# Optimization experiments

Measured on AMD Instinct MI355X. Metric: run time of the kernel, lower is better.

Reference implementation:

```python
import jax, jax.numpy as jnp
import numpy as np

N = 50000       # nodes
E = 800000      # edges
D_IN, D_H, D_OUT = 64, 64, 32


def _glorot(key, fan_in, fan_out):
    lim = np.sqrt(6.0 / (fan_in + fan_out)).astype(np.float32)
    return jax.random.uniform(key, (fan_in, fan_out), jnp.float32, -lim, lim)


def setup_inputs() -> dict:
    key = jax.random.key(0)
    k = jax.random.split(key, 4)
    x = jax.random.normal(k[0], (N, D_IN), jnp.float32)
    edge_index = jax.random.randint(k[1], (2, E), 0, N, dtype=jnp.int64)
    W1 = _glorot(k[2], D_IN, D_H)
    b1 = jnp.zeros((D_H,), jnp.float32)
    W2 = _glorot(k[3], D_H, D_OUT)
    b2 = jnp.zeros((D_OUT,), jnp.float32)
    return {"x": x, "edge_index": edge_index, "W1": W1, "b1": b1, "W2": W2, "b2": b2}


def gcn_layer(x, W, b, src, dst, n):
    # PyG GCNConv: h = XW; add self-loops (weight 1); symmetric normalization
    # out[j] = sum_{i->j} h[i] / sqrt(deg(i) deg(j)) + h[j]/deg(j) + b
    h = x @ W                                           # [n, d_out]
    deg = jax.ops.segment_sum(jnp.ones((src.shape[0],), h.dtype), dst,
                              num_segments=n) + 1.0     # in-degree + self-loop
    dinv = jax.lax.rsqrt(deg)                           # deg >= 1
    norm = (dinv[src] * dinv[dst])[:, None]             # [E, 1]
    agg = jax.ops.segment_sum(h[src] * norm, dst, num_segments=n)
    # self-loop contribution: dinv[i]*dinv[i]*h[i]
    return agg + h * (dinv * dinv)[:, None] + b


def reference(x, edge_index, W1, b1, W2, b2):
    src, dst = edge_index[0], edge_index[1]
    h = gcn_layer(x, W1, b1, src, dst, N)
    h = jax.nn.relu(h)                                  # dropout is identity in eval mode
    return gcn_layer(h, W2, b2, src, dst, N)
```

## Files before the change

### kernel.cpp

```cpp
#include <hip/hip_runtime.h>
#include <hip/hip_fp16.h>
#include <cstddef>
#include <cstdint>

namespace {

constexpr int N  = 50000;
constexpr int E  = 800000;
constexpr int DH = 64;
constexpr int DO = 32;
constexpr int NB = (N + 255) / 256;
static_assert(N < 65536, "src packed as u16");
static_assert(NB <= 256, "phase-B single tile");

__device__ inline uint16_t f2bf(float f) {
    union { float f; uint32_t u; } c; c.f = f;
    uint32_t r = c.u + 0x7FFFu + ((c.u >> 16) & 1u);
    return (uint16_t)(r >> 16);
}
__device__ inline void bf2x(uint32_t p, float& a, float& b) {
    union { uint32_t u; float f; } c0, c1;
    c0.u = p << 16; c1.u = p & 0xFFFF0000u;
    a = c0.f; b = c1.f;
}

__global__ void k_zero(int* __restrict__ cnt) {
    int i = blockIdx.x * blockDim.x + threadIdx.x;
    if (i < N) cnt[i] = 0;
}

__global__ void k_count(const int* __restrict__ dst, int* __restrict__ cnt,
                        int* __restrict__ rank) {
    int e = blockIdx.x * blockDim.x + threadIdx.x;
    if (e < E) rank[e] = atomicAdd(&cnt[dst[e]], 1);
}

__launch_bounds__(256)
__global__ void k_gemm1(const float* __restrict__ X, const float* __restrict__ W1,
                        uint16_t* __restrict__ h1) {
    __shared__ float Ws[64 * DH];
    __shared__ float Xs[64 * 68];

    const int tid = threadIdx.x;
    const int rowBase = blockIdx.x * 64;

#pragma unroll
    for (int i = 0; i < 4; ++i) {
        const int q = tid + i * 256;
        reinterpret_cast<float4*>(Ws)[q] = reinterpret_cast<const float4*>(W1)[q];
    }
#pragma unroll
    for (int i = 0; i < 4; ++i) {
        const int q   = tid + i * 256;
        const int row = q >> 4;
        const int kq  = q & 15;
        const int gr  = min(rowBase + row, N - 1);
        const float4 v = *reinterpret_cast<const float4*>(X + (size_t)gr * 64 + kq * 4);
        *reinterpret_cast<float4*>(&Xs[row * 68 + kq * 4]) = v;
    }
    __syncthreads();

    const int rg = tid >> 4;
    const int cg = tid & 15;
    float acc[4][4];
#pragma unroll
    for (int r = 0; r < 4; ++r)
#pragma unroll
        for (int c = 0; c < 4; ++c) acc[r][c] = 0.0f;

#pragma unroll
    for (int k4 = 0; k4 < 16; ++k4) {
        const int k = k4 * 4;
        float xr[4][4];
#pragma unroll
        for (int r = 0; r < 4; ++r) {
            const float4 v = *reinterpret_cast<const float4*>(&Xs[(rg * 4 + r) * 68 + k]);
            xr[r][0] = v.x; xr[r][1] = v.y; xr[r][2] = v.z; xr[r][3] = v.w;
        }
#pragma unroll
        for (int i = 0; i < 4; ++i) {
            const float4 v = *reinterpret_cast<const float4*>(&Ws[(k + i) * DH + cg * 4]);
            const float wv[4] = {v.x, v.y, v.z, v.w};
#pragma unroll
            for (int r = 0; r < 4; ++r)
#pragma unroll
                for (int c = 0; c < 4; ++c) acc[r][c] += xr[r][i] * wv[c];
        }
    }

#pragma unroll
    for (int r = 0; r < 4; ++r) {
        const int row = rowBase + rg * 4 + r;
        if (row < N) {
            uint2 o;
            o.x = (uint32_t)f2bf(acc[r][0]) | ((uint32_t)f2bf(acc[r][1]) << 16);
            o.y = (uint32_t)f2bf(acc[r][2]) | ((uint32_t)f2bf(acc[r][3]) << 16);
            *reinterpret_cast<uint2*>(&h1[(size_t)row * DH + cg * 4]) = o;
        }
    }
}

__global__ void k_scanA(const int* __restrict__ cnt, int* __restrict__ incl,
                        int* __restrict__ bsum) {
    __shared__ int ts[256];
    const int t = threadIdx.x;
    const int i = blockIdx.x * 256 + t;
    const int v = (i < N) ? cnt[i] : 0;
    ts[t] = v;
    __syncthreads();
#pragma unroll
    for (int off = 1; off < 256; off <<= 1) {
        const int u = (t >= off) ? ts[t - off] : 0;
        __syncthreads();
        ts[t] += u;
        __syncthreads();
    }
    if (i < N) incl[i] = ts[t];
    if (t == 255) bsum[blockIdx.x] = ts[255];
}

__global__ void k_scanB(int* __restrict__ bsum) {
    __shared__ int ts[256];
    const int t = threadIdx.x;
    const int v = (t < NB) ? bsum[t] : 0;
    ts[t] = v;
    __syncthreads();
#pragma unroll
    for (int off = 1; off < 256; off <<= 1) {
        const int u = (t >= off) ? ts[t - off] : 0;
        __syncthreads();
        ts[t] += u;
        __syncthreads();
    }
    if (t < NB) bsum[t] = ts[t] - v;
}

__global__ void k_scanC(const int* __restrict__ cnt, const int* __restrict__ incl,
                        const int* __restrict__ bbase, int* __restrict__ rowptr,
                        float* __restrict__ dinv) {
    const int i = blockIdx.x * 256 + threadIdx.x;
    if (i >= N) return;
    const int c    = cnt[i];
    const int excl = bbase[blockIdx.x] + incl[i] - c;
    rowptr[i] = excl;
    dinv[i]   = rsqrtf((float)(c + 1));
    if (i == N - 1) rowptr[N] = excl + c;
}

__global__ void k_fill(const int* __restrict__ src, const int* __restrict__ dst,
                       const int* __restrict__ rank, const int* __restrict__ rowptr,
                       const float* __restrict__ dinv, uint32_t* __restrict__ epack) {
    int e = blockIdx.x * blockDim.x + threadIdx.x;
    if (e >= E) return;
    const int s = src[e], d = dst[e];
    const int pos = rowptr[d] + rank[e];
    const float wn = dinv[s] * dinv[d];
    const uint16_t hb = __half_as_ushort(__float2half(wn));
    epack[pos] = (uint32_t)s | ((uint32_t)hb << 16);
}

__launch_bounds__(256)
__global__ void k_agg1(const int* __restrict__ rowptr, const uint32_t* __restrict__ epack,
                       const uint16_t* __restrict__ h1, const float* __restrict__ dinv,
                       const float* __restrict__ W2, const float* __restrict__ b1,
                       uint16_t* __restrict__ h2) {
    const int gtid = blockIdx.x * 256 + threadIdx.x;
    const int n    = gtid >> 6;
    const int lane = threadIdx.x & 63;
    if (n >= N) return;
    const int g  = lane >> 3;
    const int sl = lane & 7;

    float w2r[8][4];
#pragma unroll
    for (int k = 0; k < 8; ++k) {
        const float4 v = *reinterpret_cast<const float4*>(W2 + (size_t)(sl * 8 + k) * DO + g * 4);
        w2r[k][0] = v.x; w2r[k][1] = v.y; w2r[k][2] = v.z; w2r[k][3] = v.w;
    }
    float b1r[8];
    {
        const float4 a = *reinterpret_cast<const float4*>(b1 + sl * 8);
        const float4 b = *reinterpret_cast<const float4*>(b1 + sl * 8 + 4);
        b1r[0] = a.x; b1r[1] = a.y; b1r[2] = a.z; b1r[3] = a.w;
        b1r[4] = b.x; b1r[5] = b.y; b1r[6] = b.z; b1r[7] = b.w;
    }

    const int beg = rowptr[n], end = rowptr[n + 1];

    float acc[8] = {0.f, 0.f, 0.f, 0.f, 0.f, 0.f, 0.f, 0.f};
    for (int j = beg; j < end; j += 8) {
        const int jj = j + g;
        int s = 0; float wn = 0.0f;
        if (jj < end) {
            const uint32_t w = epack[jj];
            s  = (int)(w & 0xFFFFu);
            wn = __half2float(__ushort_as_half((uint16_t)(w >> 16)));
        }
        const uint4 v = *reinterpret_cast<const uint4*>(h1 + (size_t)s * DH + sl * 8);
        float f0, f1;
        bf2x(v.x, f0, f1); acc[0] += wn * f0; acc[1] += wn * f1;
        bf2x(v.y, f0, f1); acc[2] += wn * f0; acc[3] += wn * f1;
        bf2x(v.z, f0, f1); acc[4] += wn * f0; acc[5] += wn * f1;
        bf2x(v.w, f0, f1); acc[6] += wn * f0; acc[7] += wn * f1;
    }
#pragma unroll
    for (int m = 8; m < 64; m <<= 1)
#pragma unroll
        for (int k = 0; k < 8; ++k) acc[k] += __shfl_xor(acc[k], m);

    const float di = dinv[n], d2 = di * di;
    const uint4 sv = *reinterpret_cast<const uint4*>(h1 + (size_t)n * DH + sl * 8);
    float y[8];
    {
        float f0, f1;
        bf2x(sv.x, f0, f1); y[0] = acc[0] + f0 * d2; y[1] = acc[1] + f1 * d2;
        bf2x(sv.y, f0, f1); y[2] = acc[2] + f0 * d2; y[3] = acc[3] + f1 * d2;
        bf2x(sv.z, f0, f1); y[4] = acc[4] + f0 * d2; y[5] = acc[5] + f1 * d2;
        bf2x(sv.w, f0, f1); y[6] = acc[6] + f0 * d2; y[7] = acc[7] + f1 * d2;
    }
#pragma unroll
    for (int k = 0; k < 8; ++k) y[k] = fmaxf(y[k] + b1r[k], 0.0f);

    float o[4] = {0.f, 0.f, 0.f, 0.f};
#pragma unroll
    for (int k = 0; k < 8; ++k)
#pragma unroll
        for (int c = 0; c < 4; ++c) o[c] += y[k] * w2r[k][c];
#pragma unroll
    for (int m = 1; m < 8; m <<= 1)
#pragma unroll
        for (int c = 0; c < 4; ++c) o[c] += __shfl_xor(o[c], m);

    if (sl == 0) {
        uint2 pk;
        pk.x = (uint32_t)f2bf(o[0]) | ((uint32_t)f2bf(o[1]) << 16);
        pk.y = (uint32_t)f2bf(o[2]) | ((uint32_t)f2bf(o[3]) << 16);
        *reinterpret_cast<uint2*>(h2 + (size_t)n * DO + g * 4) = pk;
    }
}

__global__ void k_agg2(const int* __restrict__ rowptr, const uint32_t* __restrict__ epack,
                       const uint16_t* __restrict__ h2, const float* __restrict__ dinv,
                       const float* __restrict__ b2, float* __restrict__ out) {
    const int gtid = blockIdx.x * blockDim.x + threadIdx.x;
    const int n    = gtid >> 6;
    const int lane = gtid & 63;
    if (n >= N) return;
    const int g  = lane >> 2;
    const int sl = lane & 3;
    const int beg = rowptr[n], end = rowptr[n + 1];

    float acc[8] = {0.f, 0.f, 0.f, 0.f, 0.f, 0.f, 0.f, 0.f};
    for (int j = beg; j < end; j += 16) {
        const int jj = j + g;
        int s = 0; float wn = 0.0f;
        if (jj < end) {
            const uint32_t w = epack[jj];
            s  = (int)(w & 0xFFFFu);
            wn = __half2float(__ushort_as_half((uint16_t)(w >> 16)));
        }
        const uint4 v = *reinterpret_cast<const uint4*>(h2 + (size_t)s * DO + sl * 8);
        float f0, f1;
        bf2x(v.x, f0, f1); acc[0] += wn * f0; acc[1] += wn * f1;
        bf2x(v.y, f0, f1); acc[2] += wn * f0; acc[3] += wn * f1;
        bf2x(v.z, f0, f1); acc[4] += wn * f0; acc[5] += wn * f1;
        bf2x(v.w, f0, f1); acc[6] += wn * f0; acc[7] += wn * f1;
    }
#pragma unroll
    for (int m = 4; m < 64; m <<= 1)
#pragma unroll
        for (int k = 0; k < 8; ++k) acc[k] += __shfl_xor(acc[k], m);

    if (g < 2) {
        const float di = dinv[n], d2 = di * di;
        const int fb = sl * 8 + g * 4;
        const uint2 sv = *reinterpret_cast<const uint2*>(h2 + (size_t)n * DO + fb);
        float s0, s1, s2, s3;
        bf2x(sv.x, s0, s1); bf2x(sv.y, s2, s3);
        const float4 bv = *reinterpret_cast<const float4*>(b2 + fb);
        float4 o;
        o.x = acc[g * 4 + 0] + s0 * d2 + bv.x;
        o.y = acc[g * 4 + 1] + s1 * d2 + bv.y;
        o.z = acc[g * 4 + 2] + s2 * d2 + bv.z;
        o.w = acc[g * 4 + 3] + s3 * d2 + bv.w;
        *reinterpret_cast<float4*>(out + (size_t)n * DO + fb) = o;
    }
}

template <typename T>
T* alignp(char*& p, size_t count) {
    uintptr_t u = ((uintptr_t)p + 63) & ~(uintptr_t)63;
    p = (char*)(u + count * sizeof(T));
    return (T*)u;
}

}

extern "C" void kernel_launch(void* const* d_in, const int* in_sizes, int n_in,
                              void* d_out, int out_size, void* d_ws, size_t ws_size,
                              hipStream_t stream) {
    const float* x   = (const float*)d_in[0];
    const int*   ei  = (const int*)d_in[1];
    const float* W1  = (const float*)d_in[2];
    const float* b1  = (const float*)d_in[3];
    const float* W2  = (const float*)d_in[4];
    const float* b2  = (const float*)d_in[5];
    float* out = (float*)d_out;

    const int* src = ei;
    const int* dst = ei + E;

    char* p = (char*)d_ws;
    int*      cnt    = alignp<int>(p, N);
    int*      rowptr = alignp<int>(p, N + 1);
    int*      rank   = alignp<int>(p, E);
    float*    dinv   = alignp<float>(p, N);
    int*      incl   = alignp<int>(p, N);
    int*      bsum   = alignp<int>(p, NB);
    uint32_t* epack  = alignp<uint32_t>(p, E);
    uint16_t* h1     = alignp<uint16_t>(p, (size_t)N * DH);
    uint16_t* h2     = alignp<uint16_t>(p, (size_t)N * DO);

    hipLaunchKernelGGL(k_zero, dim3((N + 255) / 256), dim3(256), 0, stream, cnt);
    hipLaunchKernelGGL(k_count, dim3((E + 255) / 256), dim3(256), 0, stream,
                       dst, cnt, rank);
    hipLaunchKernelGGL(k_gemm1, dim3((N + 63) / 64), dim3(256), 0, stream, x, W1, h1);
    hipLaunchKernelGGL(k_scanA, dim3(NB), dim3(256), 0, stream, cnt, incl, bsum);
    hipLaunchKernelGGL(k_scanB, dim3(1), dim3(256), 0, stream, bsum);
    hipLaunchKernelGGL(k_scanC, dim3(NB), dim3(256), 0, stream, cnt, incl, bsum,
                       rowptr, dinv);
    hipLaunchKernelGGL(k_fill, dim3((E + 255) / 256), dim3(256), 0, stream,
                       src, dst, rank, rowptr, dinv, epack);
    hipLaunchKernelGGL(k_agg1, dim3((N * 64 + 255) / 256), dim3(256), 0, stream,
                       rowptr, epack, h1, dinv, W2, b1, h2);
    hipLaunchKernelGGL(k_agg2, dim3((N * 64 + 255) / 256), dim3(256), 0, stream,
                       rowptr, epack, h2, dinv, b2, out);
}
```

Before: 179.0 us.

## Split layer-2 GEMM out of agg1 into a separate tiled kernel

Stops fusing the W2 projection into the first aggregation kernel. agg1 now writes the ReLU activations in fp32 to a new buffer, and a new shared-memory tiled GEMM kernel multiplies them by W2 and writes h2 as bf16. This removes per-wavefront W2 register loads and shuffle reductions from the gather kernel. The cost is a 12.8 MB fp32 intermediate that must be written and read back, plus one more kernel launch.

Result: faster. 152.1 us (-15.0%).

```diff
diff --git a/kernel.cpp b/kernel.cpp
--- a/kernel.cpp
+++ b/kernel.cpp
@@ -96,6 +96,67 @@
             o.x = (uint32_t)f2bf(acc[r][0]) | ((uint32_t)f2bf(acc[r][1]) << 16);
             o.y = (uint32_t)f2bf(acc[r][2]) | ((uint32_t)f2bf(acc[r][3]) << 16);
             *reinterpret_cast<uint2*>(&h1[(size_t)row * DH + cg * 4]) = o;
+        }
+    }
+}
+
+__launch_bounds__(256)
+__global__ void k_gemm2(const float* __restrict__ Y, const float* __restrict__ W2,
+                        uint16_t* __restrict__ h2) {
+    __shared__ float Ws[64 * DO];
+    __shared__ float Xs[64 * 68];
+
+    const int tid = threadIdx.x;
+    const int rowBase = blockIdx.x * 64;
+
+#pragma unroll
+    for (int i = 0; i < 2; ++i) {
+        const int q = tid + i * 256;
+        reinterpret_cast<float4*>(Ws)[q] = reinterpret_cast<const float4*>(W2)[q];
+    }
+#pragma unroll
+    for (int i = 0; i < 4; ++i) {
+        const int q   = tid + i * 256;
+        const int row = q >> 4;
+        const int kq  = q & 15;
+        const int gr  = min(rowBase + row, N - 1);
+        const float4 v = *reinterpret_cast<const float4*>(Y + (size_t)gr * 64 + kq * 4);
+        *reinterpret_cast<float4*>(&Xs[row * 68 + kq * 4]) = v;
+    }
+    __syncthreads();
+
+    const int rg = tid >> 4;
+    const int cg = tid & 15;
+    float acc[4][2];
+#pragma unroll
+    for (int r = 0; r < 4; ++r) { acc[r][0] = 0.0f; acc[r][1] = 0.0f; }
+
+#pragma unroll
+    for (int k4 = 0; k4 < 16; ++k4) {
+        const int k = k4 * 4;
+        float xr[4][4];
+#pragma unroll
+        for (int r = 0; r < 4; ++r) {
+            const float4 v = *reinterpret_cast<const float4*>(&Xs[(rg * 4 + r) * 68 + k]);
+            xr[r][0] = v.x; xr[r][1] = v.y; xr[r][2] = v.z; xr[r][3] = v.w;
+        }
+#pragma unroll
+        for (int i = 0; i < 4; ++i) {
+            const float2 v = *reinterpret_cast<const float2*>(&Ws[(k + i) * DO + cg * 2]);
+#pragma unroll
+            for (int r = 0; r < 4; ++r) {
+                acc[r][0] += xr[r][i] * v.x;
+                acc[r][1] += xr[r][i] * v.y;
+            }
+        }
+    }
+
+#pragma unroll
+    for (int r = 0; r < 4; ++r) {
+        const int row = rowBase + rg * 4 + r;
+        if (row < N) {
+            const uint32_t o = (uint32_t)f2bf(acc[r][0]) | ((uint32_t)f2bf(acc[r][1]) << 16);
+            *reinterpret_cast<uint32_t*>(&h2[(size_t)row * DO + cg * 2]) = o;
         }
     }
 }
@@ -162,29 +223,13 @@
 __launch_bounds__(256)
 __global__ void k_agg1(const int* __restrict__ rowptr, const uint32_t* __restrict__ epack,
                        const uint16_t* __restrict__ h1, const float* __restrict__ dinv,
-                       const float* __restrict__ W2, const float* __restrict__ b1,
-                       uint16_t* __restrict__ h2) {
+                       const float* __restrict__ b1, float* __restrict__ y1) {
     const int gtid = blockIdx.x * 256 + threadIdx.x;
     const int n    = gtid >> 6;
     const int lane = threadIdx.x & 63;
     if (n >= N) return;
     const int g  = lane >> 3;
     const int sl = lane & 7;
-
-    float w2r[8][4];
-#pragma unroll
-    for (int k = 0; k < 8; ++k) {
-        const float4 v = *reinterpret_cast<const float4*>(W2 + (size_t)(sl * 8 + k) * DO + g * 4);
-        w2r[k][0] = v.x; w2r[k][1] = v.y; w2r[k][2] = v.z; w2r[k][3] = v.w;
-    }
-    float b1r[8];
-    {
-        const float4 a = *reinterpret_cast<const float4*>(b1 + sl * 8);
-        const float4 b = *reinterpret_cast<const float4*>(b1 + sl * 8 + 4);
-        b1r[0] = a.x; b1r[1] = a.y; b1r[2] = a.z; b1r[3] = a.w;
-        b1r[4] = b.x; b1r[5] = b.y; b1r[6] = b.z; b1r[7] = b.w;
-    }
-
     const int beg = rowptr[n], end = rowptr[n + 1];
 
     float acc[8] = {0.f, 0.f, 0.f, 0.f, 0.f, 0.f, 0.f, 0.f};
@@ -208,34 +253,19 @@
 #pragma unroll
         for (int k = 0; k < 8; ++k) acc[k] += __shfl_xor(acc[k], m);
 
-    const float di = dinv[n], d2 = di * di;
-    const uint4 sv = *reinterpret_cast<const uint4*>(h1 + (size_t)n * DH + sl * 8);
-    float y[8];
-    {
-        float f0, f1;
-        bf2x(sv.x, f0, f1); y[0] = acc[0] + f0 * d2; y[1] = acc[1] + f1 * d2;
-        bf2x(sv.y, f0, f1); y[2] = acc[2] + f0 * d2; y[3] = acc[3] + f1 * d2;
-        bf2x(sv.z, f0, f1); y[4] = acc[4] + f0 * d2; y[5] = acc[5] + f1 * d2;
-        bf2x(sv.w, f0, f1); y[6] = acc[6] + f0 * d2; y[7] = acc[7] + f1 * d2;
-    }
-#pragma unroll
-    for (int k = 0; k < 8; ++k) y[k] = fmaxf(y[k] + b1r[k], 0.0f);
-
-    float o[4] = {0.f, 0.f, 0.f, 0.f};
-#pragma unroll
-    for (int k = 0; k < 8; ++k)
-#pragma unroll
-        for (int c = 0; c < 4; ++c) o[c] += y[k] * w2r[k][c];
-#pragma unroll
-    for (int m = 1; m < 8; m <<= 1)
-#pragma unroll
-        for (int c = 0; c < 4; ++c) o[c] += __shfl_xor(o[c], m);
-
-    if (sl == 0) {
-        uint2 pk;
-        pk.x = (uint32_t)f2bf(o[0]) | ((uint32_t)f2bf(o[1]) << 16);
-        pk.y = (uint32_t)f2bf(o[2]) | ((uint32_t)f2bf(o[3]) << 16);
-        *reinterpret_cast<uint2*>(h2 + (size_t)n * DO + g * 4) = pk;
+    if (g < 2) {
+        const float di = dinv[n], d2 = di * di;
+        const int fb = sl * 8 + g * 4;
+        const uint2 sv = *reinterpret_cast<const uint2*>(h1 + (size_t)n * DH + fb);
+        float s0, s1, s2, s3;
+        bf2x(sv.x, s0, s1); bf2x(sv.y, s2, s3);
+        const float4 bv = *reinterpret_cast<const float4*>(b1 + fb);
+        float4 o;
+        o.x = fmaxf(acc[g * 4 + 0] + s0 * d2 + bv.x, 0.f);
+        o.y = fmaxf(acc[g * 4 + 1] + s1 * d2 + bv.y, 0.f);
+        o.z = fmaxf(acc[g * 4 + 2] + s2 * d2 + bv.z, 0.f);
+        o.w = fmaxf(acc[g * 4 + 3] + s3 * d2 + bv.w, 0.f);
+        *reinterpret_cast<float4*>(y1 + (size_t)n * DH + fb) = o;
     }
 }
 
@@ -319,6 +349,7 @@
     int*      bsum   = alignp<int>(p, NB);
     uint32_t* epack  = alignp<uint32_t>(p, E);
     uint16_t* h1     = alignp<uint16_t>(p, (size_t)N * DH);
+    float*    y1     = alignp<float>(p, (size_t)N * DH);
     uint16_t* h2     = alignp<uint16_t>(p, (size_t)N * DO);
 
     hipLaunchKernelGGL(k_zero, dim3((N + 255) / 256), dim3(256), 0, stream, cnt);
@@ -332,7 +363,8 @@
     hipLaunchKernelGGL(k_fill, dim3((E + 255) / 256), dim3(256), 0, stream,
                        src, dst, rank, rowptr, dinv, epack);
     hipLaunchKernelGGL(k_agg1, dim3((N * 64 + 255) / 256), dim3(256), 0, stream,
-                       rowptr, epack, h1, dinv, W2, b1, h2);
+                       rowptr, epack, h1, dinv, b1, y1);
+    hipLaunchKernelGGL(k_gemm2, dim3((N + 63) / 64), dim3(256), 0, stream, y1, W2, h2);
     hipLaunchKernelGGL(k_agg2, dim3((N * 64 + 255) / 256), dim3(256), 0, stream,
                        rowptr, epack, h2, dinv, b2, out);
 }
```
